# Kernel tuning notes

Measured on AMD Instinct MI355X. Metric: run time of the kernel, lower is better.

The kernel has to match this reference:

```python
import jax, jax.numpy as jnp
import numpy as np


def setup_inputs() -> dict:
    B, M, N, DEG, MAX_ITER = 256, 8192, 16384, 10, 30
    key = jax.random.key(0)
    k1, k2 = jax.random.split(key)
    rng = np.random.default_rng(0)
    cols = rng.integers(0, N, size=(M, DEG))
    cols[::2, -1] = N  # dummy (padding) entries on half the check rows; index N is the dummy column
    V_c_col = jnp.asarray(cols, dtype=jnp.int32)
    V_c_row = jnp.asarray(np.repeat(np.arange(M)[:, None], DEG, axis=1), dtype=jnp.int32)
    synd = jax.random.randint(k1, (B, M), 0, 2).astype(jnp.float32)
    llr0 = jax.random.normal(k2, (B, N), dtype=jnp.float32) + 2.0  # LLRs biased toward 'no error'
    return {"synd": synd, "llr0": llr0, "V_c_row": V_c_row, "V_c_col": V_c_col, "max_iter": MAX_ITER}


def _decode(synd, llr0, V_c_row, V_c_col, max_iter):
    B, M = synd.shape
    N = llr0.shape[1]
    dtype = llr0.dtype
    mask_dummy = (V_c_col == N)            # [M, DEG]
    cols_flat = V_c_col.reshape(-1)        # [M*DEG]
    inf = jnp.asarray(jnp.inf, dtype)
    # extended variable axis: real variables + one dummy column pinned to +inf LLR
    u_init = jnp.concatenate([llr0, jnp.full((B, 1), jnp.inf, dtype)], axis=1)   # [B, N+1]
    synd_neg = jnp.where(synd == 0, 1.0, -1.0).astype(dtype)[:, V_c_row]          # [B, M, DEG]
    message0 = u_init[:, V_c_col]                                                 # [B, M, DEG]
    l_v0 = jnp.zeros((B, N + 1), dtype)
    zeros_bn = jnp.zeros((B, N + 1), dtype)
    init = (message0, l_v0, zeros_bn, zeros_bn,
            jnp.full((B,), -1, jnp.int32), jnp.zeros((B,), jnp.int32))

    def step(carry, i):
        message, l_v, e_out, l_out, num_iters, conv = carry
        # vn_update: first iteration passes initial messages through unchanged
        a = jnp.where(i == 1, message, l_v[:, V_c_col] - message)
        # cn_update: normalized min-sum, beta = 1 - 2^{-i}
        beta = jnp.asarray(1.0, dtype) - jnp.power(jnp.asarray(2.0, dtype), -(i.astype(dtype)))
        sign = jnp.sign(a)
        sign = jnp.where(sign == 0, jnp.asarray(-1.0, dtype), sign)
        q_sign = synd_neg * jnp.prod(sign, axis=2, keepdims=True)
        ab = jnp.abs(a)
        srt = jnp.sort(ab, axis=2)
        min0, min1 = srt[:, :, :1], srt[:, :, 1:2]
        min_res = jnp.where(ab == min0, min1, min0)
        b = beta * sign * q_sign * min_res
        b = jnp.where(mask_dummy[None, :, :], jnp.asarray(0.0, dtype), b)
        # llr_update: scatter-add check->variable messages onto the intrinsic LLRs
        l_v = u_init.at[:, cols_flat].add(b.reshape(B, -1))
        l_v = l_v.at[:, -1].set(inf)
        e_v = (l_v <= 0).astype(dtype)
        # syndrome estimation: parity of the estimated error over each check's support
        s_est = jnp.mod(jnp.sum(e_v[:, V_c_col], axis=2), 2.0).astype(dtype)
        ok = jnp.all(s_est == synd, axis=1) & (num_iters == -1)
        num_iters = jnp.where(ok, i.astype(jnp.int32), num_iters)
        conv = jnp.where(ok, 1, conv)
        e_out = jnp.where(ok[:, None], e_v, e_out)
        l_out = jnp.where(ok[:, None], l_v, l_out)
        return (b, l_v, e_out, l_out, num_iters, conv), None

    (message, l_v, e_out, l_out, num_iters, conv), _ = jax.lax.scan(
        step, init, jnp.arange(1, max_iter + 1))
    # rows that never converged take the final-iteration estimate
    unconv = num_iters == -1
    e_v = (l_v <= 0).astype(dtype)
    e_out = jnp.where(unconv[:, None], e_v, e_out)
    l_out = jnp.where(unconv[:, None], l_v, l_out)
    num_iters = jnp.where(unconv, max_iter, num_iters)
    # drop the dummy column, matching e_out[:, :-1] / l_out[:, :-1]
    return e_out[:, :-1], num_iters, l_out[:, :-1], conv


def reference(synd, llr0, V_c_row, V_c_col, max_iter):
    return _decode(synd, llr0, V_c_row, V_c_col, max_iter)
```

## Files before the change

### kernel.cpp

```cpp
#include <hip/hip_runtime.h>
#include <cmath>
#include <cstdint>
#include <cstddef>

#define BB 256
#define MM 8192
#define NN 16384
#define DEG 10
#define MAX_ITER 30
#define PAR_BLOCKS 64

typedef unsigned char  u8;
typedef unsigned short u16;


__global__ void k_init(int* colcnt, int* colfill, int* mm, int* niter, int* conv, int* cnt) {
    int t = blockIdx.x * blockDim.x + threadIdx.x;
    if (t < NN) { colcnt[t] = 0; colfill[t] = 0; }
    if (t < BB) { mm[t] = 0; niter[t] = -1; conv[t] = 0; }
    if (t == 0) *cnt = 0;
}

__global__ void k_transpose_f32(const float* __restrict__ in, float* __restrict__ out,
                                float* __restrict__ out2, int R, int C) {
    __shared__ float tile[64][65];
    int c0 = blockIdx.x * 64;
    int r0 = blockIdx.y * 64;
    #pragma unroll
    for (int k = 0; k < 16; k++) {
        int idx = k * 256 + threadIdx.x;
        int i = idx >> 6, j = idx & 63;
        tile[i][j] = in[(size_t)(r0 + i) * C + (c0 + j)];
    }
    __syncthreads();
    #pragma unroll
    for (int k = 0; k < 16; k++) {
        int idx = k * 256 + threadIdx.x;
        int i = idx >> 6, j = idx & 63;
        float v = tile[j][i];
        size_t o = (size_t)(c0 + i) * R + (r0 + j);
        out[o] = v;
        if (out2) out2[o] = v;
    }
}

__global__ void k_synd_t(const float* __restrict__ synd, u8* __restrict__ syndb) {
    __shared__ float tile[64][65];
    int c0 = blockIdx.x * 64;
    int r0 = blockIdx.y * 64;
    #pragma unroll
    for (int k = 0; k < 16; k++) {
        int idx = k * 256 + threadIdx.x;
        int i = idx >> 6, j = idx & 63;
        tile[i][j] = synd[(size_t)(r0 + i) * MM + (c0 + j)];
    }
    __syncthreads();
    #pragma unroll
    for (int k = 0; k < 16; k++) {
        int idx = k * 256 + threadIdx.x;
        int i = idx >> 6, j = idx & 63;
        syndb[(size_t)(c0 + i) * BB + (r0 + j)] = (tile[j][i] != 0.0f) ? 1 : 0;
    }
}

__global__ void k_hist(const int* __restrict__ vc, int* colcnt) {
    int e = blockIdx.x * 256 + threadIdx.x;
    if (e >= MM * DEG) return;
    int c = vc[e];
    if (c < NN) atomicAdd(&colcnt[c], 1);
}

__global__ void k_scan(const int* __restrict__ colcnt, int* __restrict__ colptr) {
    __shared__ int part[256];
    __shared__ int base[257];
    int t = threadIdx.x;
    int s = 0;
    for (int i = 0; i < 64; i++) s += colcnt[t * 64 + i];
    part[t] = s;
    __syncthreads();
    if (t == 0) {
        int acc = 0;
        for (int i = 0; i < 256; i++) { base[i] = acc; acc += part[i]; }
        base[256] = acc;
    }
    __syncthreads();
    int acc = base[t];
    for (int i = 0; i < 64; i++) { int c = t * 64 + i; colptr[c] = acc; acc += colcnt[c]; }
    if (t == 255) colptr[NN] = base[256];
}

__global__ void k_fill(const int* __restrict__ vc, const int* __restrict__ colptr,
                       int* colfill, int* coledges) {
    int e = blockIdx.x * 256 + threadIdx.x;
    if (e >= MM * DEG) return;
    int c = vc[e];
    if (c < NN) {
        int p = colptr[c] + atomicAdd(&colfill[c], 1);
        coledges[p] = e;
    }
}

__global__ void k_sort(const int* __restrict__ colptr, int* coledges) {
    int n = blockIdx.x * 256 + threadIdx.x;
    if (n >= NN) return;
    int p0 = colptr[n], p1 = colptr[n + 1];
    for (int i = p0 + 1; i < p1; i++) {
        int v = coledges[i];
        int j = i - 1;
        while (j >= p0 && coledges[j] > v) { coledges[j + 1] = coledges[j]; j--; }
        coledges[j + 1] = v;
    }
}


__global__ void k_check(const int* __restrict__ vc, const float* __restrict__ lv,
                        float* __restrict__ msg,
                        float* __restrict__ sv0, float* __restrict__ sv1,
                        u16* __restrict__ sbits, const u8* __restrict__ syndb,
                        float beta, int first, int has_state) {
    __shared__ int cs[DEG];
    int m = blockIdx.x, t = threadIdx.x;
    if (t < DEG) cs[t] = vc[m * DEG + t];
    __syncthreads();
    int b2 = t * 2;
    size_t mb = (size_t)m * BB + b2;

    float pv0x = 0.f, pv0y = 0.f, pv1x = 0.f, pv1y = 0.f;
    unsigned pbx = 0, pby = 0;
    if (!first && has_state) {
        float2 a0 = *(const float2*)(sv0 + mb);
        float2 a1 = *(const float2*)(sv1 + mb);
        ushort2 pb = *(const ushort2*)(sbits + mb);
        pv0x = a0.x; pv0y = a0.y; pv1x = a1.x; pv1y = a1.y;
        pbx = pb.x; pby = pb.y;
    }
    int pi0x = (pbx >> 11) & 15, pi0y = (pby >> 11) & 15;
    unsigned pqx = (pbx >> 10) & 1u, pqy = (pby >> 10) & 1u;

    float m0x = INFINITY, m1x = INFINITY, m0y = INFINITY, m1y = INFINITY;
    unsigned negx = 0, negy = 0;
    int i0x = 0, i0y = 0;

    #pragma unroll
    for (int d = 0; d < DEG; d++) {
        int c = cs[d];
        float ax, ay;
        if (c >= NN) {
            ax = INFINITY; ay = INFINITY;
        } else {
            float2 g = *(const float2*)(lv + (size_t)c * BB + b2);
            if (first) { ax = g.x; ay = g.y; }
            else if (has_state) {
                float tx = (d == pi0x) ? pv1x : pv0x;
                float ty = (d == pi0y) ? pv1y : pv0y;
                unsigned sx = pqx ^ ((pbx >> d) & 1u);
                unsigned sy = pqy ^ ((pby >> d) & 1u);
                ax = g.x - (sx ? -tx : tx);
                ay = g.y - (sy ? -ty : ty);
            } else {
                float2 mp = *(const float2*)(msg + (size_t)(m * DEG + d) * BB + b2);
                ax = g.x - mp.x; ay = g.y - mp.y;
            }
        }
        if (!(ax > 0.0f)) negx |= 1u << d;
        if (!(ay > 0.0f)) negy |= 1u << d;
        float xx = fabsf(ax), xy = fabsf(ay);
        if (xx < m0x) { m1x = m0x; m0x = xx; i0x = d; } else if (xx < m1x) m1x = xx;
        if (xy < m0y) { m1y = m0y; m0y = xy; i0y = d; } else if (xy < m1y) m1y = xy;
    }
    uchar2 sb = *(const uchar2*)(syndb + mb);
    unsigned qx = (__popc(negx) & 1u) ^ (sb.x ? 1u : 0u);
    unsigned qy = (__popc(negy) & 1u) ^ (sb.y ? 1u : 0u);
    float v0x = beta * m0x, v1x = beta * m1x;
    float v0y = beta * m0y, v1y = beta * m1y;

    if (has_state) {
        *(float2*)(sv0 + mb) = make_float2(v0x, v0y);
        *(float2*)(sv1 + mb) = make_float2(v1x, v1y);
        ushort2 nb;
        nb.x = (u16)(negx | (qx << 10) | ((unsigned)i0x << 11));
        nb.y = (u16)(negy | (qy << 10) | ((unsigned)i0y << 11));
        *(ushort2*)(sbits + mb) = nb;
    }
    #pragma unroll
    for (int d = 0; d < DEG; d++) {
        int c = cs[d];
        if (c >= NN) continue;
        float tx = (d == i0x) ? v1x : v0x;
        float ty = (d == i0y) ? v1y : v0y;
        unsigned sx = qx ^ ((negx >> d) & 1u);
        unsigned sy = qy ^ ((negy >> d) & 1u);
        *(float2*)(msg + (size_t)(m * DEG + d) * BB + b2) =
            make_float2(sx ? -tx : tx, sy ? -ty : ty);
    }
}

__global__ void k_var(const float* __restrict__ llr0t, const float* __restrict__ msg,
                      const int* __restrict__ colptr, const int* __restrict__ coledges,
                      float* __restrict__ lv, const int* __restrict__ niter) {
    int n = blockIdx.x, t = threadIdx.x, b2 = t * 2;
    int f0 = niter[b2], f1 = niter[b2 + 1];
    if (f0 != -1 && f1 != -1) return;
    float2 s = *(const float2*)(llr0t + (size_t)n * BB + b2);
    int p0 = colptr[n], p1 = colptr[n + 1];
    for (int p = p0; p < p1; p++) {
        int e = coledges[p];
        float2 mv = *(const float2*)(msg + (size_t)e * BB + b2);
        s.x += mv.x; s.y += mv.y;
    }
    float* dst = lv + (size_t)n * BB + b2;
    if (f0 == -1 && f1 == -1) *(float2*)dst = s;
    else if (f0 == -1) dst[0] = s.x;
    else dst[1] = s.y;
}

__global__ void k_parity(const int* __restrict__ vc, const float* __restrict__ lv,
                         const u8* __restrict__ syndb, int* __restrict__ niter,
                         int* __restrict__ conv, int* __restrict__ mm,
                         int* __restrict__ cnt, int it) {
    __shared__ int s_stop, s_last;
    int b = threadIdx.x;
    bool frozen = (niter[b] != -1);
    volatile int* vmm = (volatile int*)mm;

    for (int m = blockIdx.x; m < MM; m += PAR_BLOCKS) {
        if (b == 0) s_stop = 1;
        __syncthreads();
        bool flagged = frozen || (vmm[b] != 0);
        if (!flagged) s_stop = 0;
        __syncthreads();
        if (s_stop) break;
        if (!flagged) {
            unsigned par = 0;
            #pragma unroll
            for (int d = 0; d < DEG; d++) {
                int c = vc[m * DEG + d];
                if (c < NN) par ^= (lv[(size_t)c * BB + b] <= 0.0f) ? 1u : 0u;
            }
            if (par != (unsigned)syndb[(size_t)m * BB + b]) atomicOr(&mm[b], 1);
        }
    }
    __syncthreads();
    __threadfence();
    if (b == 0) {
        int tk = atomicAdd(cnt, 1);
        s_last = (tk == PAR_BLOCKS - 1) ? 1 : 0;
    }
    __syncthreads();
    if (s_last) {
        __threadfence();
        if (niter[b] == -1 && mm[b] == 0) { niter[b] = it; conv[b] = 1; }
        mm[b] = 0;
        if (b == 0) *cnt = 0;
    }
}


__global__ void k_out_e(const float* __restrict__ lv, float* __restrict__ out) {
    __shared__ float tile[64][65];
    int c0 = blockIdx.x * 64;
    int r0 = blockIdx.y * 64;
    #pragma unroll
    for (int k = 0; k < 16; k++) {
        int idx = k * 256 + threadIdx.x;
        int i = idx >> 6, j = idx & 63;
        tile[i][j] = (lv[(size_t)(r0 + i) * BB + (c0 + j)] <= 0.0f) ? 1.0f : 0.0f;
    }
    __syncthreads();
    #pragma unroll
    for (int k = 0; k < 16; k++) {
        int idx = k * 256 + threadIdx.x;
        int i = idx >> 6, j = idx & 63;
        out[(size_t)(c0 + i) * NN + (r0 + j)] = tile[j][i];
    }
}

__global__ void k_out_scalars(const int* __restrict__ niter, const int* __restrict__ conv,
                              float* __restrict__ out_ni, float* __restrict__ out_conv) {
    int b = threadIdx.x;
    int ni = niter[b];
    out_ni[b] = (float)(ni == -1 ? MAX_ITER : ni);
    out_conv[b] = (float)conv[b];
}


extern "C" void kernel_launch(void* const* d_in, const int* in_sizes, int n_in,
                              void* d_out, int out_size, void* d_ws, size_t ws_size,
                              hipStream_t stream) {
    const float* synd = (const float*)d_in[0];
    const float* llr0 = (const float*)d_in[1];
    const int* vcol   = (const int*)d_in[3];
    float* out = (float*)d_out;

    char* ws = (char*)d_ws;
    size_t off = 0;
    auto alloc = [&](size_t bytes) {
        off = (off + 255) & ~(size_t)255;
        size_t o = off; off += bytes; return o;
    };
    float* llr0t   = (float*)(ws + alloc((size_t)NN * BB * 4));
    float* lv      = (float*)(ws + alloc((size_t)NN * BB * 4));
    float* msg     = (float*)(ws + alloc((size_t)MM * DEG * BB * 4));
    u8*   syndb    = (u8*)(ws + alloc((size_t)MM * BB));
    int* coledges = (int*)(ws + alloc((size_t)MM * DEG * 4));
    int* colptr   = (int*)(ws + alloc((size_t)(NN + 1) * 4));
    int* colcnt   = (int*)(ws + alloc((size_t)NN * 4));
    int* colfill  = (int*)(ws + alloc((size_t)NN * 4));
    int* mm       = (int*)(ws + alloc((size_t)BB * 4));
    int* niter    = (int*)(ws + alloc((size_t)BB * 4));
    int* conv     = (int*)(ws + alloc((size_t)BB * 4));
    int* cnt      = (int*)(ws + alloc(256));
    size_t need_state = ((size_t)MM * BB) * (4 + 4 + 2) + 1024;
    int has_state = (off + need_state <= ws_size) ? 1 : 0;
    float* sv0 = nullptr; float* sv1 = nullptr; u16* sbits = nullptr;
    if (has_state) {
        sv0   = (float*)(ws + alloc((size_t)MM * BB * 4));
        sv1   = (float*)(ws + alloc((size_t)MM * BB * 4));
        sbits = (u16*)(ws + alloc((size_t)MM * BB * 2));
    }
    (void)in_sizes; (void)n_in; (void)out_size;

    k_init<<<NN / 256, 256, 0, stream>>>(colcnt, colfill, mm, niter, conv, cnt);
    k_transpose_f32<<<dim3(NN / 64, BB / 64), 256, 0, stream>>>(llr0, llr0t, lv, BB, NN);
    k_synd_t<<<dim3(MM / 64, BB / 64), 256, 0, stream>>>(synd, syndb);
    k_hist<<<(MM * DEG + 255) / 256, 256, 0, stream>>>(vcol, colcnt);
    k_scan<<<1, 256, 0, stream>>>(colcnt, colptr);
    k_fill<<<(MM * DEG + 255) / 256, 256, 0, stream>>>(vcol, colptr, colfill, coledges);
    k_sort<<<NN / 256, 256, 0, stream>>>(colptr, coledges);

    for (int i = 1; i <= MAX_ITER; i++) {
        float beta = 1.0f - ldexpf(1.0f, -i);
        k_check<<<MM, 128, 0, stream>>>(vcol, lv, msg, sv0, sv1, sbits, syndb,
                                        beta, (i == 1) ? 1 : 0, has_state);
        k_var<<<NN, 128, 0, stream>>>(llr0t, msg, colptr, coledges, lv, niter);
        k_parity<<<PAR_BLOCKS, 256, 0, stream>>>(vcol, lv, syndb, niter, conv, mm, cnt, i);
    }

    size_t off_e = 0;
    size_t off_ni = (size_t)BB * NN;
    size_t off_l = off_ni + BB;
    size_t off_c = off_l + (size_t)BB * NN;
    k_out_e<<<dim3(BB / 64, NN / 64), 256, 0, stream>>>(lv, out + off_e);
    k_transpose_f32<<<dim3(BB / 64, NN / 64), 256, 0, stream>>>(lv, out + off_l, nullptr, NN, BB);
    k_out_scalars<<<1, 256, 0, stream>>>(niter, conv, out + off_ni, out + off_c);
}
```

Before: 2.007 ms.

## Drop materialized edge messages; reconstruct from compressed check state in variable update

The check kernel no longer writes the per-edge message array (M*DEG*B floats). It stores only the compressed min-sum state: two scaled minima, sign bits, parity and argmin index per check. The variable kernel rebuilds each incoming message from that state, decoding the edge index into check and slot with a multiply-shift division. This removes a large write stream per iteration at the cost of extra gathers and ALU work in the variable kernel. The compressed state buffers are now always allocated, and the workspace-size fallback path is removed.

```diff
diff --git a/kernel.cpp b/kernel.cpp
--- a/kernel.cpp
+++ b/kernel.cpp
@@ -114,10 +114,9 @@
 
 
 __global__ void k_check(const int* __restrict__ vc, const float* __restrict__ lv,
-                        float* __restrict__ msg,
                         float* __restrict__ sv0, float* __restrict__ sv1,
                         u16* __restrict__ sbits, const u8* __restrict__ syndb,
-                        float beta, int first, int has_state) {
+                        float beta, int first) {
     __shared__ int cs[DEG];
     int m = blockIdx.x, t = threadIdx.x;
     if (t < DEG) cs[t] = vc[m * DEG + t];
@@ -127,7 +126,7 @@
 
     float pv0x = 0.f, pv0y = 0.f, pv1x = 0.f, pv1y = 0.f;
     unsigned pbx = 0, pby = 0;
-    if (!first && has_state) {
+    if (!first) {
         float2 a0 = *(const float2*)(sv0 + mb);
         float2 a1 = *(const float2*)(sv1 + mb);
         ushort2 pb = *(const ushort2*)(sbits + mb);
@@ -150,16 +149,13 @@
         } else {
             float2 g = *(const float2*)(lv + (size_t)c * BB + b2);
             if (first) { ax = g.x; ay = g.y; }
-            else if (has_state) {
+            else {
                 float tx = (d == pi0x) ? pv1x : pv0x;
                 float ty = (d == pi0y) ? pv1y : pv0y;
                 unsigned sx = pqx ^ ((pbx >> d) & 1u);
                 unsigned sy = pqy ^ ((pby >> d) & 1u);
                 ax = g.x - (sx ? -tx : tx);
                 ay = g.y - (sy ? -ty : ty);
-            } else {
-                float2 mp = *(const float2*)(msg + (size_t)(m * DEG + d) * BB + b2);
-                ax = g.x - mp.x; ay = g.y - mp.y;
             }
         }
         if (!(ax > 0.0f)) negx |= 1u << d;
@@ -171,31 +167,18 @@
     uchar2 sb = *(const uchar2*)(syndb + mb);
     unsigned qx = (__popc(negx) & 1u) ^ (sb.x ? 1u : 0u);
     unsigned qy = (__popc(negy) & 1u) ^ (sb.y ? 1u : 0u);
-    float v0x = beta * m0x, v1x = beta * m1x;
-    float v0y = beta * m0y, v1y = beta * m1y;
-
-    if (has_state) {
-        *(float2*)(sv0 + mb) = make_float2(v0x, v0y);
-        *(float2*)(sv1 + mb) = make_float2(v1x, v1y);
-        ushort2 nb;
-        nb.x = (u16)(negx | (qx << 10) | ((unsigned)i0x << 11));
-        nb.y = (u16)(negy | (qy << 10) | ((unsigned)i0y << 11));
-        *(ushort2*)(sbits + mb) = nb;
-    }
-    #pragma unroll
-    for (int d = 0; d < DEG; d++) {
-        int c = cs[d];
-        if (c >= NN) continue;
-        float tx = (d == i0x) ? v1x : v0x;
-        float ty = (d == i0y) ? v1y : v0y;
-        unsigned sx = qx ^ ((negx >> d) & 1u);
-        unsigned sy = qy ^ ((negy >> d) & 1u);
-        *(float2*)(msg + (size_t)(m * DEG + d) * BB + b2) =
-            make_float2(sx ? -tx : tx, sy ? -ty : ty);
-    }
-}
-
-__global__ void k_var(const float* __restrict__ llr0t, const float* __restrict__ msg,
+
+    *(float2*)(sv0 + mb) = make_float2(beta * m0x, beta * m0y);
+    *(float2*)(sv1 + mb) = make_float2(beta * m1x, beta * m1y);
+    ushort2 nb;
+    nb.x = (u16)(negx | (qx << 10) | ((unsigned)i0x << 11));
+    nb.y = (u16)(negy | (qy << 10) | ((unsigned)i0y << 11));
+    *(ushort2*)(sbits + mb) = nb;
+}
+
+__global__ void k_var(const float* __restrict__ llr0t,
+                      const float* __restrict__ sv0, const float* __restrict__ sv1,
+                      const u16* __restrict__ sbits,
                       const int* __restrict__ colptr, const int* __restrict__ coledges,
                       float* __restrict__ lv, const int* __restrict__ niter) {
     int n = blockIdx.x, t = threadIdx.x, b2 = t * 2;
@@ -205,8 +188,18 @@
     int p0 = colptr[n], p1 = colptr[n + 1];
     for (int p = p0; p < p1; p++) {
         int e = coledges[p];
-        float2 mv = *(const float2*)(msg + (size_t)e * BB + b2);
-        s.x += mv.x; s.y += mv.y;
+        int m = (int)(((long long)e * 0x66666667LL) >> 34);
+        int d = e - m * DEG;
+        size_t mb = (size_t)m * BB + b2;
+        float2 v0 = *(const float2*)(sv0 + mb);
+        float2 v1 = *(const float2*)(sv1 + mb);
+        ushort2 bb = *(const ushort2*)(sbits + mb);
+        float tx = (d == ((bb.x >> 11) & 15)) ? v1.x : v0.x;
+        float ty = (d == ((bb.y >> 11) & 15)) ? v1.y : v0.y;
+        unsigned sx = ((bb.x >> 10) ^ (bb.x >> d)) & 1u;
+        unsigned sy = ((bb.y >> 10) ^ (bb.y >> d)) & 1u;
+        s.x += sx ? -tx : tx;
+        s.y += sy ? -ty : ty;
     }
     float* dst = lv + (size_t)n * BB + b2;
     if (f0 == -1 && f1 == -1) *(float2*)dst = s;
@@ -298,10 +291,12 @@
         off = (off + 255) & ~(size_t)255;
         size_t o = off; off += bytes; return o;
     };
-    float* llr0t   = (float*)(ws + alloc((size_t)NN * BB * 4));
-    float* lv      = (float*)(ws + alloc((size_t)NN * BB * 4));
-    float* msg     = (float*)(ws + alloc((size_t)MM * DEG * BB * 4));
-    u8*   syndb    = (u8*)(ws + alloc((size_t)MM * BB));
+    float* llr0t  = (float*)(ws + alloc((size_t)NN * BB * 4));
+    float* lv     = (float*)(ws + alloc((size_t)NN * BB * 4));
+    float* sv0    = (float*)(ws + alloc((size_t)MM * BB * 4));
+    float* sv1    = (float*)(ws + alloc((size_t)MM * BB * 4));
+    u16*   sbits  = (u16*)(ws + alloc((size_t)MM * BB * 2));
+    u8*   syndb   = (u8*)(ws + alloc((size_t)MM * BB));
     int* coledges = (int*)(ws + alloc((size_t)MM * DEG * 4));
     int* colptr   = (int*)(ws + alloc((size_t)(NN + 1) * 4));
     int* colcnt   = (int*)(ws + alloc((size_t)NN * 4));
@@ -310,15 +305,7 @@
     int* niter    = (int*)(ws + alloc((size_t)BB * 4));
     int* conv     = (int*)(ws + alloc((size_t)BB * 4));
     int* cnt      = (int*)(ws + alloc(256));
-    size_t need_state = ((size_t)MM * BB) * (4 + 4 + 2) + 1024;
-    int has_state = (off + need_state <= ws_size) ? 1 : 0;
-    float* sv0 = nullptr; float* sv1 = nullptr; u16* sbits = nullptr;
-    if (has_state) {
-        sv0   = (float*)(ws + alloc((size_t)MM * BB * 4));
-        sv1   = (float*)(ws + alloc((size_t)MM * BB * 4));
-        sbits = (u16*)(ws + alloc((size_t)MM * BB * 2));
-    }
-    (void)in_sizes; (void)n_in; (void)out_size;
+    (void)in_sizes; (void)n_in; (void)out_size; (void)ws_size;
 
     k_init<<<NN / 256, 256, 0, stream>>>(colcnt, colfill, mm, niter, conv, cnt);
     k_transpose_f32<<<dim3(NN / 64, BB / 64), 256, 0, stream>>>(llr0, llr0t, lv, BB, NN);
@@ -330,9 +317,9 @@
 
     for (int i = 1; i <= MAX_ITER; i++) {
         float beta = 1.0f - ldexpf(1.0f, -i);
-        k_check<<<MM, 128, 0, stream>>>(vcol, lv, msg, sv0, sv1, sbits, syndb,
-                                        beta, (i == 1) ? 1 : 0, has_state);
-        k_var<<<NN, 128, 0, stream>>>(llr0t, msg, colptr, coledges, lv, niter);
+        k_check<<<MM, 128, 0, stream>>>(vcol, lv, sv0, sv1, sbits, syndb,
+                                        beta, (i == 1) ? 1 : 0);
+        k_var<<<NN, 128, 0, stream>>>(llr0t, sv0, sv1, sbits, colptr, coledges, lv, niter);
         k_parity<<<PAR_BLOCKS, 256, 0, stream>>>(vcol, lv, syndb, niter, conv, mm, cnt, i);
     }
 
```

New measurement: 2.031 ms. No clear change (+1.2%).
